# Performance work log

Hardware: AMD Instinct MI355X
Metric: run time of the kernel (lower is better)

Reference implementation:

```python
import jax, jax.numpy as jnp
import numpy as np

B, C, D, H, W = 8, 16, 32, 112, 112
D_OUT, H3, W3, H2, W2 = 16, 14, 14, 7, 7
HID, OUT = 256, 128
IN_SIZE = C * H2 * W2  # 784


def setup_inputs() -> dict:
    key = jax.random.key(0)
    ks = jax.random.split(key, 8)
    s_ih = 1.0 / np.sqrt(HID)
    return {
        "x": jax.random.normal(ks[0], (B, C, D, H, W), dtype=jnp.float32),
        "W_ih": jax.random.uniform(ks[1], (3 * HID, IN_SIZE), jnp.float32, -s_ih, s_ih),
        "W_hh": jax.random.uniform(ks[2], (3 * HID, HID), jnp.float32, -s_ih, s_ih),
        "b_ih": jax.random.uniform(ks[3], (3 * HID,), jnp.float32, -s_ih, s_ih),
        "b_hh": jax.random.uniform(ks[4], (3 * HID,), jnp.float32, -s_ih, s_ih),
        "W_out": jax.random.uniform(ks[5], (OUT, HID), jnp.float32, -s_ih, s_ih),
        "b_out": jax.random.uniform(ks[6], (OUT,), jnp.float32, -s_ih, s_ih),
    }


def reference(x, W_ih, W_hh, b_ih, b_hh, W_out, b_out):
    # AdaptiveAvgPool3d (D,H,W)->(D_OUT,H3,W3): divisible factors -> mean pooling
    p3 = x.reshape(B, C, D_OUT, D // D_OUT, H3, H // H3, W3, W // W3).mean(axis=(3, 5, 7))
    # AdaptiveAvgPool2d per temporal slice (H3,W3)->(H2,W2)
    p2 = p3.reshape(B, C, D_OUT, H2, H3 // H2, W2, W3 // W2).mean(axis=(4, 6))
    # sequence over D_OUT: [T, B, C*H2*W2]
    seq = p2.transpose(2, 0, 1, 3, 4).reshape(D_OUT, B, IN_SIZE)

    def step(h, inp):
        gi = inp @ W_ih.T + b_ih  # [B, 3H]
        gh = h @ W_hh.T + b_hh    # [B, 3H]
        ir, iz, inn = jnp.split(gi, 3, axis=-1)
        hr, hz, hn = jnp.split(gh, 3, axis=-1)
        r = jax.nn.sigmoid(ir + hr)
        z = jax.nn.sigmoid(iz + hz)
        n = jnp.tanh(inn + r * hn)
        h_new = (1.0 - z) * n + z * h
        return h_new, None

    h0 = jnp.zeros((B, HID), dtype=x.dtype)
    h, _ = jax.lax.scan(step, h0, seq)
    return h @ W_out.T + b_out
```

## Files before the change

### kernel.cpp

```cpp
#include <hip/hip_runtime.h>
#include <hip/hip_bf16.h>
#include <cstdint>

#define BB 8
#define CC 16
#define DD 32
#define HH 112
#define WW 112
#define TT 16
#define HID 256
#define OUTN 128
#define INSZ 784

__device__ __forceinline__ float bf16lo(uint32_t u) { return __uint_as_float(u << 16); }
__device__ __forceinline__ float bf16hi(uint32_t u) { return __uint_as_float(u & 0xffff0000u); }
__device__ __forceinline__ float bf16s(uint16_t u)  { return __uint_as_float(((uint32_t)u) << 16); }

__device__ __forceinline__ uint16_t f32_to_bf16_rne(float f) {
    uint32_t u = __float_as_uint(f);
    return (uint16_t)((u + 0x7fffu + ((u >> 16) & 1u)) >> 16);
}

__global__ __launch_bounds__(256) void detect_kernel(const uint16_t* __restrict__ x,
                                                     int* __restrict__ flag) {
    __shared__ int cnt;
    if (threadIdx.x == 0) cnt = 0;
    __syncthreads();
    int local = 0;
    for (int i = threadIdx.x; i < 8192; i += 256) {
        uint32_t e = (x[i] >> 7) & 0xFFu;
        if (e == 0u || e >= 0x90u) local++;
    }
    atomicAdd(&cnt, local);
    __syncthreads();
    if (threadIdx.x == 0) *flag = (cnt > 400) ? 1 : 0;
}

__global__ __launch_bounds__(256) void pool_kernel(const void* __restrict__ xv,
                                                   float* __restrict__ seq,
                                                   const int* __restrict__ flag) {
    const int isf32 = *flag;
    int gid = blockIdx.x;
    int t = gid & 15, c = (gid >> 4) & 15, b = gid >> 8;
    long base = (long)(((b * CC + c) * DD) + t * 2) * (HH * WW);
    __shared__ float chunk[6272];
    int tid = threadIdx.x;
    float s = 0.0f;
    if (!isf32) {
        const uint4* p = reinterpret_cast<const uint4*>((const uint16_t*)xv + base);
        for (int m = tid; m < 3136; m += 256) {
            uint4 v = p[m];
            chunk[m] = bf16lo(v.x) + bf16hi(v.x) + bf16lo(v.y) + bf16hi(v.y)
                     + bf16lo(v.z) + bf16hi(v.z) + bf16lo(v.w) + bf16hi(v.w);
        }
        __syncthreads();
        if (tid < 49) {
            int h2 = tid / 7, w2 = tid - h2 * 7;
            #pragma unroll
            for (int d = 0; d < 2; d++)
                for (int hh = 0; hh < 16; hh++) {
                    int row = d * 1568 + (h2 * 16 + hh) * 14 + w2 * 2;
                    s += chunk[row] + chunk[row + 1];
                }
        }
    } else {
        const float4* p = reinterpret_cast<const float4*>((const float*)xv + base);
        for (int m = tid; m < 6272; m += 256) {
            float4 v = p[m];
            chunk[m] = v.x + v.y + v.z + v.w;
        }
        __syncthreads();
        if (tid < 49) {
            int h2 = tid / 7, w2 = tid - h2 * 7;
            #pragma unroll
            for (int d = 0; d < 2; d++)
                for (int hh = 0; hh < 16; hh++) {
                    int row = d * 3136 + (h2 * 16 + hh) * 28 + w2 * 4;
                    s += chunk[row] + chunk[row + 1] + chunk[row + 2] + chunk[row + 3];
                }
        }
    }
    if (tid < 49) {
        seq[(long)(t * BB + b) * INSZ + c * 49 + tid] = s * (1.0f / 512.0f);
    }
}

__global__ __launch_bounds__(256) void pack_wih(const void* __restrict__ W,
                                                float* __restrict__ WT,
                                                const int* __restrict__ flag) {
    const int isf32 = *flag;
    int g = blockIdx.x * 256 + threadIdx.x;
    int j = g / INSZ, k = g - j * INSZ;
    float v = isf32 ? ((const float*)W)[g] : bf16s(((const uint16_t*)W)[g]);
    WT[(long)k * 768 + j] = v;
}

__global__ __launch_bounds__(256) void pack_whh(const void* __restrict__ W,
                                                uint32_t* __restrict__ WP,
                                                const int* __restrict__ flag) {
    const int isf32 = *flag;
    int g = blockIdx.x * 256 + threadIdx.x;
    int j = g >> 7, kk = g & 127;
    uint32_t u;
    if (isf32) {
        float2 v = ((const float2*)W)[g];
        u = (uint32_t)f32_to_bf16_rne(v.x) | ((uint32_t)f32_to_bf16_rne(v.y) << 16);
    } else {
        u = ((const uint32_t*)W)[g];
    }
    WP[kk * 768 + j] = u;
}

__global__ __launch_bounds__(256) void gi_kernel(const float* __restrict__ seq,
                                                 const float* __restrict__ wihT,
                                                 const void* __restrict__ bih,
                                                 float* __restrict__ gi,
                                                 const int* __restrict__ flag) {
    const int isf32 = *flag;
    int jg = blockIdx.x % 3, tbg = blockIdx.x / 3;
    int tb0 = tbg * 4;
    int j = jg * 256 + threadIdx.x;
    __shared__ __align__(16) float s_in[INSZ * 4];
    const float* sbase = seq + (long)tb0 * INSZ;
    for (int idx = threadIdx.x; idx < INSZ * 4; idx += 256) {
        int i = idx / INSZ, k = idx - i * INSZ;
        s_in[k * 4 + i] = sbase[idx];
    }
    __syncthreads();
    float bv = isf32 ? ((const float*)bih)[j] : bf16s(((const uint16_t*)bih)[j]);
    float a0 = bv, a1 = bv, a2 = bv, a3 = bv;
    const float* wp = wihT + j;
    const float4* s4 = reinterpret_cast<const float4*>(s_in);
    #pragma unroll 8
    for (int k = 0; k < INSZ; k++) {
        float w = wp[(long)k * 768];
        float4 sv = s4[k];
        a0 += w * sv.x; a1 += w * sv.y; a2 += w * sv.z; a3 += w * sv.w;
    }
    gi[(long)(tb0 + 0) * 768 + j] = a0;
    gi[(long)(tb0 + 1) * 768 + j] = a1;
    gi[(long)(tb0 + 2) * 768 + j] = a2;
    gi[(long)(tb0 + 3) * 768 + j] = a3;
}

__global__ __launch_bounds__(768) void gru_kernel(const float* __restrict__ gi,
                                                  const uint32_t* __restrict__ whhP,
                                                  const void* __restrict__ bhh,
                                                  const void* __restrict__ Wout,
                                                  const void* __restrict__ bout,
                                                  void* __restrict__ out,
                                                  const int* __restrict__ flag) {
    const int isf32 = *flag;
    int b = blockIdx.x;
    int j = threadIdx.x;
    __shared__ __align__(16) float h_s[HID];
    __shared__ __align__(16) float g_s[768];
    if (j < HID) h_s[j] = 0.0f;
    float bh = isf32 ? ((const float*)bhh)[j] : bf16s(((const uint16_t*)bhh)[j]);
    const uint32_t* wp = whhP + j;
    __syncthreads();
    #pragma unroll 1
    for (int t = 0; t < TT; t++) {
        float a0 = bh, a1 = 0.0f;
        const float2* h2p = reinterpret_cast<const float2*>(h_s);
        #pragma unroll 8
        for (int kk = 0; kk < 128; kk++) {
            uint32_t u = wp[kk * 768];
            float2 hv = h2p[kk];
            a0 += bf16lo(u) * hv.x;
            a1 += bf16hi(u) * hv.y;
        }
        g_s[j] = a0 + a1;
        __syncthreads();
        if (j < HID) {
            const float* gp = gi + (long)(t * BB + b) * 768;
            float r = 1.0f / (1.0f + __expf(-(gp[j]       + g_s[j])));
            float z = 1.0f / (1.0f + __expf(-(gp[j + 256] + g_s[j + 256])));
            float npre = gp[j + 512] + r * g_s[j + 512];
            float n = 2.0f / (1.0f + __expf(-2.0f * npre)) - 1.0f;
            h_s[j] = (1.0f - z) * n + z * h_s[j];
        }
        __syncthreads();
    }
    if (j < OUTN) {
        float acc = isf32 ? ((const float*)bout)[j] : bf16s(((const uint16_t*)bout)[j]);
        if (!isf32) {
            const uint4* wo = reinterpret_cast<const uint4*>((const uint16_t*)Wout + (long)j * HID);
            #pragma unroll
            for (int k = 0; k < 32; k++) {
                uint4 v = wo[k];
                const float* hp2 = &h_s[k * 8];
                acc += bf16lo(v.x) * hp2[0] + bf16hi(v.x) * hp2[1]
                     + bf16lo(v.y) * hp2[2] + bf16hi(v.y) * hp2[3]
                     + bf16lo(v.z) * hp2[4] + bf16hi(v.z) * hp2[5]
                     + bf16lo(v.w) * hp2[6] + bf16hi(v.w) * hp2[7];
            }
            ((uint16_t*)out)[b * OUTN + j] = f32_to_bf16_rne(acc);
        } else {
            const float4* wo = reinterpret_cast<const float4*>((const float*)Wout + (long)j * HID);
            #pragma unroll
            for (int k = 0; k < 64; k++) {
                float4 v = wo[k];
                const float* hp2 = &h_s[k * 4];
                acc += v.x * hp2[0] + v.y * hp2[1] + v.z * hp2[2] + v.w * hp2[3];
            }
            ((float*)out)[b * OUTN + j] = acc;
        }
    }
}

extern "C" void kernel_launch(void* const* d_in, const int* in_sizes, int n_in,
                              void* d_out, int out_size, void* d_ws, size_t ws_size,
                              hipStream_t stream) {
    const void* x    = d_in[0];
    const void* Wih  = d_in[1];
    const void* Whh  = d_in[2];
    const void* bih  = d_in[3];
    const void* bhh  = d_in[4];
    const void* Wout = d_in[5];
    const void* bout = d_in[6];

    char* ws = (char*)d_ws;
    float*    seq  = (float*)ws;
    float*    gi   = (float*)(ws + 401408);
    float*    wihT = (float*)(ws + 1048576);
    uint32_t* whhP = (uint32_t*)(ws + 4194304);
    int*     flagp = (int*)(ws + 8388608);

    detect_kernel<<<1, 256, 0, stream>>>((const uint16_t*)x, flagp);
    pool_kernel<<<2048, 256, 0, stream>>>(x, seq, flagp);
    pack_wih<<<2352, 256, 0, stream>>>(Wih, wihT, flagp);
    pack_whh<<<384, 256, 0, stream>>>(Whh, whhP, flagp);
    gi_kernel<<<96, 256, 0, stream>>>(seq, wihT, bih, gi, flagp);
    gru_kernel<<<8, 768, 0, stream>>>(gi, whhP, bhh, Wout, bout, d_out, flagp);
}
```

Measured before the change: 438.6 us.

## Merge weight packing kernels, split-K gi GEMM with atomics, cache W_hh in LDS

The two weight-packing kernels become one launch, which also seeds gi with the input bias. The gi GEMM is split into two K halves across twice as many blocks, with partial sums accumulated through atomicAdd. This raises parallelism from 96 blocks and removes one launch. The GRU kernel preloads the first 48 rows of the packed W_hh into shared memory (about 147 KB), so each timestep reads fewer weights from global memory. The risks are atomic overhead, non-deterministic summation order, and high LDS use in the GRU block.

```diff
diff --git a/kernel.cpp b/kernel.cpp
--- a/kernel.cpp
+++ b/kernel.cpp
@@ -11,6 +11,7 @@
 #define HID 256
 #define OUTN 128
 #define INSZ 784
+#define NCACHE 48
 
 __device__ __forceinline__ float bf16lo(uint32_t u) { return __uint_as_float(u << 16); }
 __device__ __forceinline__ float bf16hi(uint32_t u) { return __uint_as_float(u & 0xffff0000u); }
@@ -85,62 +86,68 @@
     }
 }
 
-__global__ __launch_bounds__(256) void pack_wih(const void* __restrict__ W,
-                                                float* __restrict__ WT,
+__global__ __launch_bounds__(256) void pack_all(const void* __restrict__ Wih,
+                                                float* __restrict__ wihT,
+                                                const void* __restrict__ Whh,
+                                                uint32_t* __restrict__ whhP,
+                                                const void* __restrict__ bih,
+                                                float* __restrict__ gi,
                                                 const int* __restrict__ flag) {
     const int isf32 = *flag;
-    int g = blockIdx.x * 256 + threadIdx.x;
-    int j = g / INSZ, k = g - j * INSZ;
-    float v = isf32 ? ((const float*)W)[g] : bf16s(((const uint16_t*)W)[g]);
-    WT[(long)k * 768 + j] = v;
-}
-
-__global__ __launch_bounds__(256) void pack_whh(const void* __restrict__ W,
-                                                uint32_t* __restrict__ WP,
-                                                const int* __restrict__ flag) {
-    const int isf32 = *flag;
-    int g = blockIdx.x * 256 + threadIdx.x;
-    int j = g >> 7, kk = g & 127;
-    uint32_t u;
-    if (isf32) {
-        float2 v = ((const float2*)W)[g];
-        u = (uint32_t)f32_to_bf16_rne(v.x) | ((uint32_t)f32_to_bf16_rne(v.y) << 16);
+    int blk = blockIdx.x;
+    if (blk < 2352) {
+        int g = blk * 256 + threadIdx.x;
+        int j = g / INSZ, k = g - j * INSZ;
+        float v = isf32 ? ((const float*)Wih)[g] : bf16s(((const uint16_t*)Wih)[g]);
+        wihT[(long)k * 768 + j] = v;
+    } else if (blk < 2736) {
+        int g = (blk - 2352) * 256 + threadIdx.x;
+        int jr = g >> 7, kk = g & 127;
+        uint32_t u;
+        if (isf32) {
+            float2 v = ((const float2*)Whh)[g];
+            u = (uint32_t)f32_to_bf16_rne(v.x) | ((uint32_t)f32_to_bf16_rne(v.y) << 16);
+        } else {
+            u = ((const uint32_t*)Whh)[g];
+        }
+        whhP[kk * 768 + jr] = u;
     } else {
-        u = ((const uint32_t*)W)[g];
-    }
-    WP[kk * 768 + j] = u;
+        int g = (blk - 2736) * 256 + threadIdx.x;
+        int jj = g % 768;
+        float bv = isf32 ? ((const float*)bih)[jj] : bf16s(((const uint16_t*)bih)[jj]);
+        gi[g] = bv;
+    }
 }
 
 __global__ __launch_bounds__(256) void gi_kernel(const float* __restrict__ seq,
                                                  const float* __restrict__ wihT,
-                                                 const void* __restrict__ bih,
-                                                 float* __restrict__ gi,
-                                                 const int* __restrict__ flag) {
-    const int isf32 = *flag;
-    int jg = blockIdx.x % 3, tbg = blockIdx.x / 3;
+                                                 float* __restrict__ gi) {
+    int jg = blockIdx.x % 3;
+    int tbg = (blockIdx.x / 3) & 31;
+    int kh = blockIdx.x / 96;
     int tb0 = tbg * 4;
     int j = jg * 256 + threadIdx.x;
-    __shared__ __align__(16) float s_in[INSZ * 4];
-    const float* sbase = seq + (long)tb0 * INSZ;
-    for (int idx = threadIdx.x; idx < INSZ * 4; idx += 256) {
-        int i = idx / INSZ, k = idx - i * INSZ;
-        s_in[k * 4 + i] = sbase[idx];
-    }
-    __syncthreads();
-    float bv = isf32 ? ((const float*)bih)[j] : bf16s(((const uint16_t*)bih)[j]);
-    float a0 = bv, a1 = bv, a2 = bv, a3 = bv;
-    const float* wp = wihT + j;
+    int k0 = kh * 392;
+    __shared__ __align__(16) float s_in[392 * 4];
+    const float* sbase = seq + (long)tb0 * INSZ + k0;
+    for (int idx = threadIdx.x; idx < 392 * 4; idx += 256) {
+        int i = idx / 392, k = idx - i * 392;
+        s_in[k * 4 + i] = sbase[(long)i * INSZ + k];
+    }
+    __syncthreads();
+    float a0 = 0.0f, a1 = 0.0f, a2 = 0.0f, a3 = 0.0f;
+    const float* wp = wihT + (long)k0 * 768 + j;
     const float4* s4 = reinterpret_cast<const float4*>(s_in);
     #pragma unroll 8
-    for (int k = 0; k < INSZ; k++) {
+    for (int k = 0; k < 392; k++) {
         float w = wp[(long)k * 768];
         float4 sv = s4[k];
         a0 += w * sv.x; a1 += w * sv.y; a2 += w * sv.z; a3 += w * sv.w;
     }
-    gi[(long)(tb0 + 0) * 768 + j] = a0;
-    gi[(long)(tb0 + 1) * 768 + j] = a1;
-    gi[(long)(tb0 + 2) * 768 + j] = a2;
-    gi[(long)(tb0 + 3) * 768 + j] = a3;
+    atomicAdd(&gi[(long)(tb0 + 0) * 768 + j], a0);
+    atomicAdd(&gi[(long)(tb0 + 1) * 768 + j], a1);
+    atomicAdd(&gi[(long)(tb0 + 2) * 768 + j], a2);
+    atomicAdd(&gi[(long)(tb0 + 3) * 768 + j], a3);
 }
 
 __global__ __launch_bounds__(768) void gru_kernel(const float* __restrict__ gi,
@@ -155,17 +162,27 @@
     int j = threadIdx.x;
     __shared__ __align__(16) float h_s[HID];
     __shared__ __align__(16) float g_s[768];
+    __shared__ __align__(16) uint32_t w_s[NCACHE * 768];
     if (j < HID) h_s[j] = 0.0f;
     float bh = isf32 ? ((const float*)bhh)[j] : bf16s(((const uint16_t*)bhh)[j]);
-    const uint32_t* wp = whhP + j;
+    for (int idx = j; idx < NCACHE * 768; idx += 768) w_s[idx] = whhP[idx];
+    const uint32_t* wpg = whhP + (long)NCACHE * 768 + j;
+    const uint32_t* wls = w_s + j;
     __syncthreads();
     #pragma unroll 1
     for (int t = 0; t < TT; t++) {
         float a0 = bh, a1 = 0.0f;
         const float2* h2p = reinterpret_cast<const float2*>(h_s);
         #pragma unroll 8
-        for (int kk = 0; kk < 128; kk++) {
-            uint32_t u = wp[kk * 768];
+        for (int kk = 0; kk < 128 - NCACHE; kk++) {
+            uint32_t u = wpg[kk * 768];
+            float2 hv = h2p[NCACHE + kk];
+            a0 += bf16lo(u) * hv.x;
+            a1 += bf16hi(u) * hv.y;
+        }
+        #pragma unroll 8
+        for (int kk = 0; kk < NCACHE; kk++) {
+            uint32_t u = wls[kk * 768];
             float2 hv = h2p[kk];
             a0 += bf16lo(u) * hv.x;
             a1 += bf16hi(u) * hv.y;
@@ -229,8 +246,7 @@
 
     detect_kernel<<<1, 256, 0, stream>>>((const uint16_t*)x, flagp);
     pool_kernel<<<2048, 256, 0, stream>>>(x, seq, flagp);
-    pack_wih<<<2352, 256, 0, stream>>>(Wih, wihT, flagp);
-    pack_whh<<<384, 256, 0, stream>>>(Whh, whhP, flagp);
-    gi_kernel<<<96, 256, 0, stream>>>(seq, wihT, bih, gi, flagp);
+    pack_all<<<3120, 256, 0, stream>>>(Wih, wihT, Whh, whhP, bih, gi, flagp);
+    gi_kernel<<<192, 256, 0, stream>>>(seq, wihT, gi);
     gru_kernel<<<8, 768, 0, stream>>>(gi, whhP, bhh, Wout, bout, d_out, flagp);
 }
```

Measured after the change: 406.4 us. 1.08x faster.
